# Kernel tuning notes

Measured on AMD Instinct MI355X. Metric: run time of the kernel, lower is better.

## Reference

```python
import jax, jax.numpy as jnp
import numpy as np

H, HK, D, BLK, GH = 32, 8, 96, 64, 128   # q heads, kv heads, head_dim, gate block, gate hidden
HIDDEN = 3072
THR = 0.03
NEG = -1e30

def _rot_half(x):
    h = x.shape[-1] // 2
    return jnp.concatenate([-x[..., h:], x[..., :h]], axis=-1)

def setup_inputs() -> dict:
    key = jax.random.key(0)
    ks = jax.random.split(key, 6)
    B, S = 1, 2048
    hidden_states = jax.random.normal(ks[0], (B, S, HIDDEN), dtype=jnp.float32)
    # RoPE tables, theta = 10000
    inv_freq = 1.0 / (10000.0 ** (np.arange(0, D, 2, dtype=np.float32) / D))
    t = np.arange(S, dtype=np.float32)
    freqs = np.outer(t, inv_freq)                   # [S, D/2]
    emb = np.concatenate([freqs, freqs], axis=-1)   # [S, D]
    cos = jnp.asarray(np.cos(emb), dtype=jnp.float32)
    sin = jnp.asarray(np.sin(emb), dtype=jnp.float32)
    op = H * D + 2 * HK * D
    qkv_w = jax.random.normal(ks[1], (HIDDEN, op), dtype=jnp.float32) * 0.02
    o_w = jax.random.normal(ks[2], (H * D, HIDDEN), dtype=jnp.float32) * 0.02
    gate_wq = jax.random.normal(ks[3], (D, GH), dtype=jnp.float32) * 0.05
    gate_wk = jax.random.normal(ks[4], (2 * D, GH), dtype=jnp.float32) * 0.05
    return dict(hidden_states=hidden_states, cos=cos, sin=sin,
                qkv_w=qkv_w, o_w=o_w, gate_wq=gate_wq, gate_wk=gate_wk)

def reference(hidden_states, cos, sin, qkv_w, o_w, gate_wq, gate_wk):
    B, S, _ = hidden_states.shape
    G = H // HK            # GQA group size
    nB = S // BLK          # number of gate blocks
    scale = D ** -0.5

    # fused QKV projection and head split
    qkv = hidden_states @ qkv_w
    q = qkv[..., : H * D].reshape(B, S, H, D)
    k = qkv[..., H * D : H * D + HK * D].reshape(B, S, HK, D)
    v = qkv[..., H * D + HK * D :].reshape(B, S, HK, D)
    q_nope, k_nope = q, k

    # RoPE (unsqueeze over head dim)
    cs = cos[None, :, None, :]
    sn = sin[None, :, None, :]
    q = q * cs + _rot_half(q) * sn
    k = k * cs + _rot_half(k) * sn

    # ---- learned block-sparse gate (SeerAttention AttnGate) ----
    kb = k_nope.reshape(B, nB, BLK, HK, D)
    k_pool = jnp.concatenate([kb.mean(2), kb.max(2)], axis=-1)      # [B,nB,HK,2D] avg+max seq pooling
    k_gate = jnp.einsum('bnhe,eg->bnhg', k_pool, gate_wk)
    q_pool = q_nope.reshape(B, S, HK, G, D).mean(3)                 # q-head pooling to kv heads
    q_pool = q_pool.reshape(B, nB, BLK, HK, D).mean(2)              # block pooling
    q_gate = jnp.einsum('bnhd,dg->bnhg', q_pool, gate_wq)
    gate_logits = jnp.einsum('bqhg,bkhg->bhqk', q_gate, k_gate) * (GH ** -0.5)
    blk_causal = jnp.tril(jnp.ones((nB, nB), dtype=bool))
    gate_logits = jnp.where(blk_causal, gate_logits, NEG)
    gate_probs = jax.nn.softmax(gate_logits, axis=-1)
    block_mask = (gate_probs >= THR) & blk_causal                   # threshold sparsity method
    block_mask = block_mask | jnp.eye(nB, dtype=bool)               # diagonal block always active

    # expand block mask to token level, intersect with causal mask
    tok_mask = jnp.repeat(jnp.repeat(block_mask, BLK, axis=2), BLK, axis=3)  # [B,HK,S,S]
    causal = jnp.tril(jnp.ones((S, S), dtype=bool))
    mask = tok_mask & causal

    # ---- block-sparse masked attention with GQA ----
    qh = q.transpose(0, 2, 1, 3).reshape(B, HK, G, S, D)
    kh = k.transpose(0, 2, 1, 3)                                    # [B,HK,S,D]
    vh = v.transpose(0, 2, 1, 3)
    scores = jnp.einsum('bhgsd,bhtd->bhgst', qh, kh) * scale
    scores = jnp.where(mask[:, :, None], scores, NEG)
    attn = jax.nn.softmax(scores, axis=-1)
    out = jnp.einsum('bhgst,bhtd->bhgsd', attn, vh)                 # [B,HK,G,S,D]
    out = out.reshape(B, H, S, D).transpose(0, 2, 1, 3).reshape(B, S, H * D)
    return out @ o_w
```

## Files before the change

kernel.cpp:

```cpp
#include <hip/hip_runtime.h>
#include <hip/hip_bf16.h>
#include <math.h>

#define S_LEN 2048
#define HID 3072
#define NHEAD 32
#define NKV 8
#define HDIM 96
#define QKV_N 4608
#define NB 32
#define GHDIM 128
#define KOFF 3072
#define VOFF 3840

typedef __attribute__((ext_vector_type(8))) short bf16x8;
typedef __attribute__((ext_vector_type(4))) short bf16x4;
typedef __attribute__((ext_vector_type(4))) float f32x4;
typedef unsigned short ushort_t;

#define SCALE2 0.14724444754f

__device__ __forceinline__ unsigned short f2bf(float x) {
    unsigned u = __float_as_uint(x);
    u += 0x7fffu + ((u >> 16) & 1u);
    return (unsigned short)(u >> 16);
}
__device__ __forceinline__ unsigned packbf2(float a, float b) {
    return (unsigned)f2bf(a) | ((unsigned)f2bf(b) << 16);
}
__device__ __forceinline__ float bf2f(ushort_t u) {
    return __uint_as_float(((unsigned)u) << 16);
}

#define GLOBAL_AS __attribute__((address_space(1)))
#define LDS_AS __attribute__((address_space(3)))
__device__ __forceinline__ void gl_lds16(const void* g, void* l) {
    __builtin_amdgcn_global_load_lds((const GLOBAL_AS unsigned int*)g,
                                     (LDS_AS unsigned int*)l, 16, 0, 0);
}
__device__ __forceinline__ void barrier_raw() {
    asm volatile("s_barrier" ::: "memory");
}

__global__ __launch_bounds__(256, 4) void gemm_bf16(const ushort_t* __restrict__ A,
                                                    const ushort_t* __restrict__ Bt,
                                                    float* __restrict__ C,
                                                    ushort_t* __restrict__ Cbf,
                                                    float* __restrict__ CfK,
                                                    int M, int N, int K, int mode) {
    __shared__ ushort_t As[128 * 64];
    __shared__ ushort_t Bs[128 * 64];
    const int tid = threadIdx.x;
    const int lane = tid & 63;
    const int w = tid >> 6;
    const int wm = (w >> 1) * 64;
    const int wn = (w & 1) * 64;
    const int l15 = lane & 15;
    const int quad = lane >> 4;
    const int m0 = blockIdx.y * 128;
    const int n0 = blockIdx.x * 128;

    f32x4 acc[4][4] = {};

    for (int k0 = 0; k0 < K; k0 += 64) {
        __syncthreads();
#pragma unroll
        for (int j = 0; j < 4; ++j) {
            int s = j * 256 + w * 64 + lane;
            int row = s >> 3;
            int kc = (s & 7) ^ (row & 7);
            gl_lds16(A + (size_t)(m0 + row) * K + k0 + kc * 8,
                     &As[(j * 256 + w * 64) * 8]);
        }
#pragma unroll
        for (int j = 0; j < 4; ++j) {
            int s = j * 256 + w * 64 + lane;
            int row = s >> 3;
            int kc = (s & 7) ^ (row & 7);
            gl_lds16(Bt + (size_t)(n0 + row) * K + k0 + kc * 8,
                     &Bs[(j * 256 + w * 64) * 8]);
        }
        __syncthreads();
        bf16x8 af[2][4], bf[2][4];
#pragma unroll
        for (int mt = 0; mt < 4; ++mt) {
            int row = wm + mt * 16 + l15;
            int rx = row & 7;
#pragma unroll
            for (int ph = 0; ph < 2; ++ph)
                af[ph][mt] = *(const bf16x8*)&As[(row * 8 + ((ph * 4 + quad) ^ rx)) * 8];
        }
#pragma unroll
        for (int nt = 0; nt < 4; ++nt) {
            int row = wn + nt * 16 + l15;
            int rx = row & 7;
#pragma unroll
            for (int ph = 0; ph < 2; ++ph)
                bf[ph][nt] = *(const bf16x8*)&Bs[(row * 8 + ((ph * 4 + quad) ^ rx)) * 8];
        }
#pragma unroll
        for (int ph = 0; ph < 2; ++ph)
#pragma unroll
            for (int mt = 0; mt < 4; ++mt)
#pragma unroll
                for (int nt = 0; nt < 4; ++nt)
                    acc[mt][nt] = __builtin_amdgcn_mfma_f32_16x16x32_bf16(
                        af[ph][mt], bf[ph][nt], acc[mt][nt], 0, 0, 0);
    }
    if (mode == 0) {
#pragma unroll
        for (int mt = 0; mt < 4; ++mt)
#pragma unroll
            for (int nt = 0; nt < 4; ++nt)
#pragma unroll
                for (int r = 0; r < 4; ++r) {
                    int row = m0 + wm + mt * 16 + quad * 4 + r;
                    int col = n0 + wn + nt * 16 + l15;
                    C[(size_t)row * N + col] = acc[mt][nt][r];
                }
    } else {
        const bool isK = (n0 >= KOFF) && (n0 < VOFF);
#pragma unroll
        for (int mt = 0; mt < 4; ++mt)
#pragma unroll
            for (int nt = 0; nt < 4; ++nt)
#pragma unroll
                for (int r = 0; r < 4; ++r) {
                    int row = m0 + wm + mt * 16 + quad * 4 + r;
                    int col = n0 + wn + nt * 16 + l15;
                    Cbf[(size_t)row * N + col] = f2bf(acc[mt][nt][r]);
                    if (isK) CfK[(size_t)row * 768 + col - KOFF] = acc[mt][nt][r];
                }
    }
}

__device__ __forceinline__ void conv_body(const float* __restrict__ X,
                                          ushort_t* __restrict__ Y, int i) {
    const float4 v = *(const float4*)(X + (size_t)i * 4);
    int2 p;
    p.x = (int)packbf2(v.x, v.y);
    p.y = (int)packbf2(v.z, v.w);
    *(int2*)(Y + (size_t)i * 4) = p;
}

__device__ __forceinline__ void transpose_body(const float* __restrict__ W,
                                               ushort_t* __restrict__ Wt,
                                               int K, int N, int k0, int n0, int tid) {
    __shared__ float Ts[64][65];
    {
        int r = tid >> 2, cq = tid & 3;
#pragma unroll
        for (int i = 0; i < 4; ++i) {
            int c = cq * 16 + i * 4;
            const float4 v = *(const float4*)(W + (size_t)(k0 + r) * N + n0 + c);
            Ts[r][c] = v.x; Ts[r][c + 1] = v.y; Ts[r][c + 2] = v.z; Ts[r][c + 3] = v.w;
        }
    }
    __syncthreads();
#pragma unroll
    for (int it = 0; it < 2; ++it) {
        int n = (tid >> 3) + it * 32;
        int kc = tid & 7;
        int4 r;
        r.x = (int)(packbf2(Ts[kc * 8 + 0][n], Ts[kc * 8 + 1][n]));
        r.y = (int)(packbf2(Ts[kc * 8 + 2][n], Ts[kc * 8 + 3][n]));
        r.z = (int)(packbf2(Ts[kc * 8 + 4][n], Ts[kc * 8 + 5][n]));
        r.w = (int)(packbf2(Ts[kc * 8 + 6][n], Ts[kc * 8 + 7][n]));
        *(int4*)(Wt + (size_t)(n0 + n) * K + k0 + kc * 8) = r;
    }
}

__global__ __launch_bounds__(256) void prep1(const float* __restrict__ hidden,
                                             ushort_t* __restrict__ h_bf,
                                             const float* __restrict__ qkv_w,
                                             ushort_t* __restrict__ w1t) {
    int id = blockIdx.x;
    int tid = threadIdx.x;
    if (id < 6144) {
        conv_body(hidden, h_bf, id * 256 + tid);
    } else {
        int r = id - 6144;
        transpose_body(qkv_w, w1t, HID, QKV_N, (r / 72) * 64, (r % 72) * 64, tid);
    }
}

__global__ __launch_bounds__(256) void prep2(const ushort_t* __restrict__ qkv_bf,
                                             const float* __restrict__ cosb,
                                             const float* __restrict__ sinb,
                                             ushort_t* __restrict__ Qb,
                                             ushort_t* __restrict__ Kb,
                                             ushort_t* __restrict__ Vtb,
                                             const float* __restrict__ o_w,
                                             ushort_t* __restrict__ o_wt) {
    int id = blockIdx.x;
    int tid = threadIdx.x;
    if (id < 15360) {
        int idx = id * 256 + tid;
        int d = idx % 48;
        int tmp = idx / 48;
        int head = tmp % 40;
        int s = tmp / 40;
        float c0 = cosb[s * 96 + d], c1 = cosb[s * 96 + d + 48];
        float s0 = sinb[s * 96 + d], s1 = sinb[s * 96 + d + 48];
        if (head < 32) {
            size_t base = (size_t)s * QKV_N + head * 96;
            float x0 = bf2f(qkv_bf[base + d]), x1 = bf2f(qkv_bf[base + d + 48]);
            size_t ob = (size_t)s * HID + head * 96;
            Qb[ob + d] = f2bf((x0 * c0 - x1 * s0) * SCALE2);
            Qb[ob + d + 48] = f2bf((x1 * c1 + x0 * s1) * SCALE2);
        } else {
            int hh = head - 32;
            size_t base = (size_t)s * QKV_N + KOFF + hh * 96;
            float x0 = bf2f(qkv_bf[base + d]), x1 = bf2f(qkv_bf[base + d + 48]);
            size_t ob = ((size_t)hh * S_LEN + s) * 96;
            Kb[ob + d] = f2bf(x0 * c0 - x1 * s0);
            Kb[ob + d + 48] = f2bf(x1 * c1 + x0 * s1);
        }
    } else if (id < 15616) {
        int r = id - 15360;
        int ibk = r & 31, h = r >> 5;
        __shared__ ushort_t Vs[64][104];
        {
            int rr = tid >> 2, seg = tid & 3;
#pragma unroll
            for (int j = 0; j < 3; ++j) {
                int c = seg * 24 + j * 8;
                const int4 v = *(const int4*)(qkv_bf + (size_t)(ibk * 64 + rr) * QKV_N +
                                              VOFF + h * 96 + c);
                *(int4*)&Vs[rr][c] = v;
            }
        }
        __syncthreads();
#pragma unroll
        for (int it = 0; it < 3; ++it) {
            int s = tid + it * 256;
            int d = s >> 3, tc = s & 7;
            int4 o;
            o.x = (int)Vs[tc * 8 + 0][d] | ((int)Vs[tc * 8 + 1][d] << 16);
            o.y = (int)Vs[tc * 8 + 2][d] | ((int)Vs[tc * 8 + 3][d] << 16);
            o.z = (int)Vs[tc * 8 + 4][d] | ((int)Vs[tc * 8 + 5][d] << 16);
            o.w = (int)Vs[tc * 8 + 6][d] | ((int)Vs[tc * 8 + 7][d] << 16);
            *(int4*)(Vtb + ((size_t)h * 96 + d) * S_LEN + ibk * 64 + tc * 8) = o;
        }
    } else {
        int r = id - 15616;
        transpose_body(o_w, o_wt, HID, HID, (r / 48) * 64, (r % 48) * 64, tid);
    }
}

__global__ __launch_bounds__(256) void pool_gate_kernel(const float* __restrict__ qkvK,
                                                        const ushort_t* __restrict__ qkv_bf,
                                                        const float* __restrict__ gate_wk,
                                                        const float* __restrict__ gate_wq,
                                                        float* __restrict__ k_gate,
                                                        float* __restrict__ q_gate) {
    int nb = blockIdx.x, h = blockIdx.y;
    int tid = threadIdx.x;
    __shared__ float poolk[192];
    __shared__ float poolq[96];
    if (tid < 128) {
        if (tid < 96) {
            float s = 0.f, mx = -1e30f;
            for (int i = 0; i < 64; i++) {
                float v = qkvK[(size_t)(nb * 64 + i) * 768 + h * 96 + tid];
                s += v;
                mx = fmaxf(mx, v);
            }
            poolk[tid] = s * (1.f / 64.f);
            poolk[96 + tid] = mx;
        }
    } else {
        int t2 = tid - 128;
        if (t2 < 96) {
            float s = 0.f;
            for (int i = 0; i < 64; i++)
#pragma unroll
                for (int g = 0; g < 4; g++)
                    s += bf2f(qkv_bf[(size_t)(nb * 64 + i) * QKV_N + (h * 4 + g) * 96 + t2]);
            poolq[t2] = s * (1.f / 256.f);
        }
    }
    __syncthreads();
    if (tid < 128) {
        float acc = 0.f;
        for (int e = 0; e < 192; e++) acc += poolk[e] * gate_wk[e * GHDIM + tid];
        k_gate[(size_t)(nb * NKV + h) * GHDIM + tid] = acc;
    } else {
        int t2 = tid - 128;
        float acc = 0.f;
        for (int e = 0; e < 96; e++) acc += poolq[e] * gate_wq[e * GHDIM + t2];
        q_gate[(size_t)(nb * NKV + h) * GHDIM + t2] = acc;
    }
}

__global__ __launch_bounds__(64) void blockmask_kernel(const float* __restrict__ q_gate,
                                                       const float* __restrict__ k_gate,
                                                       int* __restrict__ mask) {
    int h = blockIdx.x, qb = blockIdx.y;
    int tid = threadIdx.x;
    __shared__ float logits[32];
    if (tid < 32) {
        if (tid <= qb) {
            float acc = 0.f;
            const float* qg = &q_gate[(size_t)(qb * NKV + h) * GHDIM];
            const float* kg = &k_gate[(size_t)(tid * NKV + h) * GHDIM];
            for (int e = 0; e < GHDIM; e++) acc += qg[e] * kg[e];
            logits[tid] = acc * 0.08838834764831845f;
        } else {
            logits[tid] = -1e30f;
        }
    }
    __syncthreads();
    if (tid < 32) {
        float mx = -1e30f;
        for (int j = 0; j <= qb; j++) mx = fmaxf(mx, logits[j]);
        float sum = 0.f;
        for (int j = 0; j <= qb; j++) sum += __expf(logits[j] - mx);
        float p = (tid <= qb) ? __expf(logits[tid] - mx) / sum : 0.f;
        int m = ((p >= 0.03f) && (tid <= qb)) || (tid == qb);
        mask[(h * NB + qb) * NB + tid] = m;
    }
}

__global__ __launch_bounds__(256) void attn_mfma(const ushort_t* __restrict__ Qb,
                                                 const ushort_t* __restrict__ Kb,
                                                 const ushort_t* __restrict__ Vtb,
                                                 const int* __restrict__ mask,
                                                 ushort_t* __restrict__ out) {
    const int hq = blockIdx.x;
    const int ib = NB - 1 - (int)blockIdx.y;
    const int h = hq >> 2;
    const int tid = threadIdx.x;
    const int lane = tid & 63;
    const int w = tid >> 6;
    const int l15 = lane & 15;
    const int quad = lane >> 4;

    __shared__ ushort_t KsL[2][64 * 96];
    __shared__ ushort_t VtL[2][96 * 64];

    int pk[3];
    {
        int b0 = quad + (l15 & 7);
#pragma unroll
        for (int ks = 0; ks < 3; ++ks) {
            int p = b0 + ks * 4;
            if (p >= 12) p -= 12;
            if (p >= 12) p -= 12;
            pk[ks] = p;
        }
    }

    bf16x8 qf[3];
    {
        const ushort_t* qp = Qb + (size_t)(ib * 64 + w * 16 + l15) * HID + hq * 96;
#pragma unroll
        for (int ks = 0; ks < 3; ++ks)
            qf[ks] = *(const bf16x8*)(qp + ks * 32 + quad * 8);
    }

    const ushort_t* kbase = Kb + (size_t)h * S_LEN * 96;
    const ushort_t* vbase = Vtb + (size_t)h * 96 * S_LEN;

    unsigned long long bits =
        __ballot((lane <= ib) && (mask[(h * NB + ib) * NB + (lane & 31)] != 0));

    float m_i = -1e30f, l_i = 0.f;
    f32x4 acc_o[6] = {};

    auto stage = [&](int jb, int buf) {
#pragma unroll
        for (int j = 0; j < 3; ++j) {
            int s = j * 256 + w * 64 + lane;
            int t = (s * 2731) >> 15;
            int cpos = s - t * 12;
            int c = cpos - (t & 7);
            if (c < 0) c += 12;
            gl_lds16(kbase + (size_t)(jb * 64 + t) * 96 + c * 8,
                     &KsL[buf][(j * 256 + w * 64) * 8]);
        }
#pragma unroll
        for (int j = 0; j < 3; ++j) {
            int s = j * 256 + w * 64 + lane;
            int d = s >> 3;
            int tc = (s & 7) ^ (d & 7);
            gl_lds16(vbase + (size_t)d * S_LEN + jb * 64 + tc * 8,
                     &VtL[buf][(j * 256 + w * 64) * 8]);
        }
    };

    int jb = (int)__builtin_ctzll(bits);
    bits &= bits - 1;
    stage(jb, 0);
    int cur = 0;

    while (true) {
        int jn = -1;
        if (bits) {
            jn = (int)__builtin_ctzll(bits);
            bits &= bits - 1;
        }
        if (jn >= 0) {
            stage(jn, cur ^ 1);
            asm volatile("s_waitcnt vmcnt(6)" ::: "memory");
        } else {
            asm volatile("s_waitcnt vmcnt(0)" ::: "memory");
        }
        barrier_raw();

        const ushort_t* Kc = KsL[cur];
        const ushort_t* Vc = VtL[cur];

        f32x4 st[4] = {};
#pragma unroll
        for (int ks = 0; ks < 3; ++ks)
#pragma unroll
            for (int nt = 0; nt < 4; ++nt) {
                bf16x8 kb = *(const bf16x8*)&Kc[(nt * 16 + l15) * 96 + pk[ks] * 8];
                st[nt] = __builtin_amdgcn_mfma_f32_16x16x32_bf16(kb, qf[ks], st[nt], 0, 0, 0);
            }
        if (jb == ib) {
            int q = w * 16 + l15;
#pragma unroll
            for (int nt = 0; nt < 4; ++nt)
#pragma unroll
                for (int r = 0; r < 4; ++r)
                    if ((nt * 16 + quad * 4 + r) > q) st[nt][r] = -1e30f;
        }
        float mx = -1e30f;
#pragma unroll
        for (int nt = 0; nt < 4; ++nt)
#pragma unroll
            for (int r = 0; r < 4; ++r) mx = fmaxf(mx, st[nt][r]);
        mx = fmaxf(mx, __shfl_xor(mx, 16));
        mx = fmaxf(mx, __shfl_xor(mx, 32));
        float mnew = fmaxf(m_i, mx);
        float alpha = __builtin_amdgcn_exp2f(m_i - mnew);
        float ps = 0.f;
#pragma unroll
        for (int nt = 0; nt < 4; ++nt)
#pragma unroll
            for (int r = 0; r < 4; ++r) {
                float p = __builtin_amdgcn_exp2f(st[nt][r] - mnew);
                st[nt][r] = p;
                ps += p;
            }
        ps += __shfl_xor(ps, 16);
        ps += __shfl_xor(ps, 32);
        l_i = l_i * alpha + ps;
        m_i = mnew;
#pragma unroll
        for (int t = 0; t < 6; ++t)
#pragma unroll
            for (int r = 0; r < 4; ++r) acc_o[t][r] *= alpha;
        bf16x4 pf[4];
#pragma unroll
        for (int kblk = 0; kblk < 4; ++kblk) {
            union { bf16x4 v; unsigned u[2]; } pb;
            pb.u[0] = packbf2(st[kblk][0], st[kblk][1]);
            pb.u[1] = packbf2(st[kblk][2], st[kblk][3]);
            pf[kblk] = pb.v;
        }
#pragma unroll
        for (int kblk = 0; kblk < 4; ++kblk) {
            int cchunk = kblk * 2 + (quad >> 1);
            int eoff = (quad & 1) * 4;
#pragma unroll
            for (int dt = 0; dt < 6; ++dt) {
                int d = dt * 16 + l15;
                bf16x4 vf = *(const bf16x4*)&Vc[(d * 8 + (cchunk ^ (d & 7))) * 8 + eoff];
                acc_o[dt] = __builtin_amdgcn_mfma_f32_16x16x16bf16_1k(
                    vf, pf[kblk], acc_o[dt], 0, 0, 0);
            }
        }

        if (jn < 0) break;
        asm volatile("s_waitcnt lgkmcnt(0)" ::: "memory");
        barrier_raw();
        jb = jn;
        cur ^= 1;
    }

    float inv = 1.f / l_i;
    size_t orow = (size_t)(ib * 64 + w * 16 + l15) * HID + hq * 96;
#pragma unroll
    for (int dt = 0; dt < 6; ++dt) {
        int2 pkd;
        pkd.x = (int)packbf2(acc_o[dt][0] * inv, acc_o[dt][1] * inv);
        pkd.y = (int)packbf2(acc_o[dt][2] * inv, acc_o[dt][3] * inv);
        *(int2*)(out + orow + dt * 16 + quad * 4) = pkd;
    }
}

extern "C" void kernel_launch(void* const* d_in, const int* in_sizes, int n_in,
                              void* d_out, int out_size, void* d_ws, size_t ws_size,
                              hipStream_t stream) {
    const float* hidden  = (const float*)d_in[0];
    const float* cosb    = (const float*)d_in[1];
    const float* sinb    = (const float*)d_in[2];
    const float* qkv_w   = (const float*)d_in[3];
    const float* o_w     = (const float*)d_in[4];
    const float* gate_wq = (const float*)d_in[5];
    const float* gate_wk = (const float*)d_in[6];
    float* out = (float*)d_out;

    char* ws = (char*)d_ws;
    ushort_t* qkv_bf   = (ushort_t*)ws;
    float*    qkv_f32K = (float*)(ws + 18874368);
    ushort_t* h_bf     = (ushort_t*)(ws + 25165824);
    ushort_t* w1t      = (ushort_t*)(ws + 37748736);
    ushort_t* attn_out = (ushort_t*)(ws + 66060288);
    ushort_t* Kb       = (ushort_t*)(ws + 78643200);
    ushort_t* Vtb      = (ushort_t*)(ws + 81788928);
    float*    k_gate   = (float*)(ws + 84934656);
    float*    q_gate   = (float*)(ws + 85065728);
    int*      mask     = (int*)(ws + 85196800);
    ushort_t* Qb   = h_bf;
    ushort_t* o_wt = w1t;

    prep1<<<9600, 256, 0, stream>>>(hidden, h_bf, qkv_w, w1t);
    gemm_bf16<<<dim3(QKV_N / 128, S_LEN / 128), 256, 0, stream>>>(
        h_bf, w1t, nullptr, qkv_bf, qkv_f32K, S_LEN, QKV_N, HID, 1);
    pool_gate_kernel<<<dim3(NB, NKV), 256, 0, stream>>>(qkv_f32K, qkv_bf,
                                                        gate_wk, gate_wq, k_gate, q_gate);
    blockmask_kernel<<<dim3(NKV, NB), 64, 0, stream>>>(q_gate, k_gate, mask);
    prep2<<<17920, 256, 0, stream>>>(qkv_bf, cosb, sinb, Qb, Kb, Vtb, o_w, o_wt);
    attn_mfma<<<dim3(NHEAD, NB), 256, 0, stream>>>(Qb, Kb, Vtb, mask, attn_out);
    gemm_bf16<<<dim3(HID / 128, S_LEN / 128), 256, 0, stream>>>(
        attn_out, o_wt, out, nullptr, nullptr, S_LEN, HID, HID, 0);
}
```

Baseline: 386.7 us.

## Parallelize q pooling and gate logits, add MFMA priority hints in attention

The q-head pooling in the gate kernel now spreads the 64-row reduction over 8 row-chunks with 8-wide vector loads and a shared-memory combine, instead of one scalar serial loop per thread. The block-mask kernel goes to 256 threads, with 8 lanes per key block each doing part of the dot product and a shuffle reduction. The attention kernel wraps its MFMA loops in s_setprio to favour matrix issue across waves. The small gate kernels were latency-bound, and the priority hints may or may not help scheduling.

```diff
diff --git a/kernel.cpp b/kernel.cpp
--- a/kernel.cpp
+++ b/kernel.cpp
@@ -258,6 +258,7 @@
     int tid = threadIdx.x;
     __shared__ float poolk[192];
     __shared__ float poolq[96];
+    __shared__ float poolq2[8][96];
     if (tid < 128) {
         if (tid < 96) {
             float s = 0.f, mx = -1e30f;
@@ -272,13 +273,31 @@
     } else {
         int t2 = tid - 128;
         if (t2 < 96) {
-            float s = 0.f;
-            for (int i = 0; i < 64; i++)
-#pragma unroll
-                for (int g = 0; g < 4; g++)
-                    s += bf2f(qkv_bf[(size_t)(nb * 64 + i) * QKV_N + (h * 4 + g) * 96 + t2]);
-            poolq[t2] = s * (1.f / 256.f);
-        }
+            int o = t2 % 12;
+            int hf = t2 / 12;
+            float part[8] = {};
+            for (int ii = 0; ii < 8; ++ii) {
+                int i = hf * 8 + ii;
+                const ushort_t* rp = qkv_bf + (size_t)(nb * 64 + i) * QKV_N +
+                                     h * 4 * 96 + o * 8;
+#pragma unroll
+                for (int g = 0; g < 4; ++g) {
+                    bf16x8 v = *(const bf16x8*)(rp + g * 96);
+#pragma unroll
+                    for (int j = 0; j < 8; ++j) part[j] += bf2f((ushort_t)v[j]);
+                }
+            }
+#pragma unroll
+            for (int j = 0; j < 8; ++j) poolq2[hf][o * 8 + j] = part[j];
+        }
+    }
+    __syncthreads();
+    if (tid >= 128 && tid < 224) {
+        int t2 = tid - 128;
+        float s = 0.f;
+#pragma unroll
+        for (int hf = 0; hf < 8; ++hf) s += poolq2[hf][t2];
+        poolq[t2] = s * (1.f / 256.f);
     }
     __syncthreads();
     if (tid < 128) {
@@ -293,23 +312,27 @@
     }
 }
 
-__global__ __launch_bounds__(64) void blockmask_kernel(const float* __restrict__ q_gate,
-                                                       const float* __restrict__ k_gate,
-                                                       int* __restrict__ mask) {
+__global__ __launch_bounds__(256) void blockmask_kernel(const float* __restrict__ q_gate,
+                                                        const float* __restrict__ k_gate,
+                                                        int* __restrict__ mask) {
     int h = blockIdx.x, qb = blockIdx.y;
     int tid = threadIdx.x;
     __shared__ float logits[32];
-    if (tid < 32) {
-        if (tid <= qb) {
-            float acc = 0.f;
-            const float* qg = &q_gate[(size_t)(qb * NKV + h) * GHDIM];
-            const float* kg = &k_gate[(size_t)(tid * NKV + h) * GHDIM];
-            for (int e = 0; e < GHDIM; e++) acc += qg[e] * kg[e];
-            logits[tid] = acc * 0.08838834764831845f;
-        } else {
-            logits[tid] = -1e30f;
-        }
-    }
+    int kb = tid >> 3, e8 = tid & 7;
+    float acc = 0.f;
+    if (kb <= qb) {
+        const float* qg = &q_gate[(size_t)(qb * NKV + h) * GHDIM];
+        const float* kg = &k_gate[(size_t)(kb * NKV + h) * GHDIM];
+#pragma unroll
+        for (int i = 0; i < 16; ++i) {
+            int e = e8 * 16 + i;
+            acc += qg[e] * kg[e];
+        }
+    }
+    acc += __shfl_xor(acc, 1);
+    acc += __shfl_xor(acc, 2);
+    acc += __shfl_xor(acc, 4);
+    if (e8 == 0) logits[kb] = (kb <= qb) ? acc * 0.08838834764831845f : -1e30f;
     __syncthreads();
     if (tid < 32) {
         float mx = -1e30f;
@@ -412,6 +435,7 @@
         const ushort_t* Vc = VtL[cur];
 
         f32x4 st[4] = {};
+        __builtin_amdgcn_s_setprio(1);
 #pragma unroll
         for (int ks = 0; ks < 3; ++ks)
 #pragma unroll
@@ -419,6 +443,7 @@
                 bf16x8 kb = *(const bf16x8*)&Kc[(nt * 16 + l15) * 96 + pk[ks] * 8];
                 st[nt] = __builtin_amdgcn_mfma_f32_16x16x32_bf16(kb, qf[ks], st[nt], 0, 0, 0);
             }
+        __builtin_amdgcn_s_setprio(0);
         if (jb == ib) {
             int q = w * 16 + l15;
 #pragma unroll
@@ -461,6 +486,7 @@
             pb.u[1] = packbf2(st[kblk][2], st[kblk][3]);
             pf[kblk] = pb.v;
         }
+        __builtin_amdgcn_s_setprio(1);
 #pragma unroll
         for (int kblk = 0; kblk < 4; ++kblk) {
             int cchunk = kblk * 2 + (quad >> 1);
@@ -473,6 +499,7 @@
                     vf, pf[kblk], acc_o[dt], 0, 0, 0);
             }
         }
+        __builtin_amdgcn_s_setprio(0);
 
         if (jn < 0) break;
         asm volatile("s_waitcnt lgkmcnt(0)" ::: "memory");
@@ -523,7 +550,7 @@
         h_bf, w1t, nullptr, qkv_bf, qkv_f32K, S_LEN, QKV_N, HID, 1);
     pool_gate_kernel<<<dim3(NB, NKV), 256, 0, stream>>>(qkv_f32K, qkv_bf,
                                                         gate_wk, gate_wq, k_gate, q_gate);
-    blockmask_kernel<<<dim3(NKV, NB), 64, 0, stream>>>(q_gate, k_gate, mask);
+    blockmask_kernel<<<dim3(NKV, NB), 256, 0, stream>>>(q_gate, k_gate, mask);
     prep2<<<17920, 256, 0, stream>>>(qkv_bf, cosb, sinb, Qb, Kb, Vtb, o_w, o_wt);
     attn_mfma<<<dim3(NHEAD, NB), 256, 0, stream>>>(Qb, Kb, Vtb, mask, attn_out);
     gemm_bf16<<<dim3(HID / 128, S_LEN / 128), 256, 0, stream>>>(
```

Result: no change. 381.8 us (-1.3%).
